# Optimization experiments

Hardware: AMD Instinct MI355X
Metric: run time of the kernel (lower is better)

The kernel has to match this reference:

```python
import jax, jax.numpy as jnp
import numpy as np

B, L, D = 8192, 2048, 256


def setup_inputs() -> dict:
    key = jax.random.key(0)
    kx, kl = jax.random.split(key)
    x = jax.random.normal(kx, (B, D), dtype=jnp.float32)
    landmarks = jax.random.normal(kl, (L, D), dtype=jnp.float32)
    return {"x": x, "landmarks": landmarks}


def reference(x, landmarks):
    # RBF layer: out[b, l] = exp(-gamma * sum_d (landmarks[l, d] - x[b, d])^2)
    # gamma='auto' -> 1 / n_features (landmarks.shape[1])
    gamma = jnp.float32(1.0 / landmarks.shape[1])
    # avoids materializing the [B, L, D] broadcast-diff intermediate)
    x2 = jnp.sum(x * x, axis=-1, keepdims=True)          # [B, 1]
    l2 = jnp.sum(landmarks * landmarks, axis=-1)         # [L]
    cross = jnp.einsum('bd,ld->bl', x, landmarks)        # [B, L]
    d2 = jnp.maximum(x2 + l2[None, :] - 2.0 * cross, 0.0)
    return jnp.exp(-gamma * d2)
```

## Files before the change

### kernel.cpp

```cpp
#include <hip/hip_runtime.h>


typedef __bf16 bf16x8 __attribute__((ext_vector_type(8)));
typedef float  f32x4  __attribute__((ext_vector_type(4)));

#define B_ROWS 8192
#define L_ROWS 2048
#define K_DIM  256

#define GLD_LDS(g, l) __builtin_amdgcn_global_load_lds(                      \
    (const __attribute__((address_space(1))) void*)(g),                      \
    (__attribute__((address_space(3))) void*)(l), 16, 0, 0)

__device__ __forceinline__ unsigned short f32_to_bf16_rne(float f) {
    union { float f; unsigned int u; } v; v.f = f;
    unsigned int u = v.u;
    unsigned int r = (u + 0x7fffu + ((u >> 16) & 1u)) >> 16;
    return (unsigned short)r;
}

__global__ __launch_bounds__(256) void cvt_rows_kernel(
    const float* __restrict__ x, const float* __restrict__ lm,
    unsigned short* __restrict__ xb, unsigned short* __restrict__ lb,
    float* __restrict__ x2, float* __restrict__ l2)
{
    const int lane = threadIdx.x & 63;
    const int gw   = blockIdx.x * 4 + (threadIdx.x >> 6);
    const float* in; unsigned short* outb; float* sq; int row;
    if (gw < B_ROWS) { in = x;  outb = xb; sq = x2; row = gw; }
    else             { in = lm; outb = lb; sq = l2; row = gw - B_ROWS; }
    const float4 v = ((const float4*)(in + (size_t)row * K_DIM))[lane];
    ushort4 o;
    o.x = f32_to_bf16_rne(v.x);
    o.y = f32_to_bf16_rne(v.y);
    o.z = f32_to_bf16_rne(v.z);
    o.w = f32_to_bf16_rne(v.w);
    ((ushort4*)(outb + (size_t)row * K_DIM))[lane] = o;
    float s = v.x*v.x + v.y*v.y + v.z*v.z + v.w*v.w;
    #pragma unroll
    for (int off = 32; off > 0; off >>= 1) s += __shfl_down(s, off, 64);
    if (lane == 0) sq[row] = s;
}

__global__ __launch_bounds__(512, 2) void rbf_gemm_kernel(
    const unsigned short* __restrict__ A,
    const unsigned short* __restrict__ Bm,
    const float* __restrict__ x2,
    const float* __restrict__ l2,
    float* __restrict__ out)
{
    __shared__ unsigned short As[2][256 * 64];
    __shared__ unsigned short Bs[2][256 * 64];

    const int tid  = threadIdx.x;
    const int wave = tid >> 6;
    const int lane = tid & 63;
    const int wm = wave >> 2;
    const int wn = wave & 3;

    const int bid = blockIdx.x;
    const int wg  = (bid & 7) * 32 + (bid >> 3);
    const int bm  = wg & 31;
    const int bn  = wg >> 5;

    f32x4 acc[8][4];
    #pragma unroll
    for (int i = 0; i < 8; ++i)
        #pragma unroll
        for (int j = 0; j < 4; ++j)
            acc[i][j] = (f32x4){0.f, 0.f, 0.f, 0.f};

    const int ldrow = lane >> 3;
    const int ldcol = (((lane & 7) ^ ldrow) * 8);

    const unsigned short* Ab = A  + (size_t)(bm * 256) * K_DIM;
    const unsigned short* Bb = Bm + (size_t)(bn * 256) * K_DIM;

#define STAGE(buf, k0)                                                       \
    _Pragma("unroll")                                                        \
    for (int it = 0; it < 4; ++it) {                                         \
        const int r = wave * 32 + it * 8;                                    \
        GLD_LDS(Ab + (r + ldrow) * K_DIM + (k0) + ldcol, &As[buf][r * 64]);  \
        GLD_LDS(Bb + (r + ldrow) * K_DIM + (k0) + ldcol, &Bs[buf][r * 64]);  \
    }

    STAGE(0, 0);

    const int xr = (lane & 7) << 4;

    #pragma unroll
    for (int t = 0; t < 4; ++t) {
        const int cur = t & 1;
        if (t < 3) { STAGE(cur ^ 1, (t + 1) * 64); }
        if (t < 3) asm volatile("s_waitcnt vmcnt(8)" ::: "memory");
        else       asm volatile("s_waitcnt vmcnt(0)" ::: "memory");
        asm volatile("s_barrier" ::: "memory");

        #pragma unroll
        for (int kk = 0; kk < 64; kk += 32) {
            const int osw = ((kk * 2 + (lane >> 4) * 16) ^ xr) >> 1;
            bf16x8 af[8], bfr[4];
            #pragma unroll
            for (int nt = 0; nt < 4; ++nt)
                bfr[nt] = *(const bf16x8*)&Bs[cur][(wn*64 + nt*16 + (lane & 15)) * 64 + osw];
            #pragma unroll
            for (int mt = 0; mt < 8; ++mt)
                af[mt]  = *(const bf16x8*)&As[cur][(wm*128 + mt*16 + (lane & 15)) * 64 + osw];
            #pragma unroll
            for (int mt = 0; mt < 8; ++mt)
                #pragma unroll
                for (int nt = 0; nt < 4; ++nt)
                    acc[mt][nt] = __builtin_amdgcn_mfma_f32_16x16x32_bf16(
                        bfr[nt], af[mt], acc[mt][nt], 0, 0, 0);
        }
        if (t < 3) asm volatile("s_barrier" ::: "memory");
    }
#undef STAGE

    const float gamma = 1.0f / 256.0f;
    const int row0 = bm * 256 + wm * 128 + (lane & 15);
    const int col0 = bn * 256 + wn * 64 + (lane >> 4) * 4;

    f32x4 lv[4];
    #pragma unroll
    for (int nt = 0; nt < 4; ++nt) lv[nt] = *(const f32x4*)&l2[col0 + nt * 16];

    #pragma unroll
    for (int mt = 0; mt < 8; ++mt) {
        const int row = row0 + mt * 16;
        const float xv = x2[row];
        const size_t rb = (size_t)row * L_ROWS;
        #pragma unroll
        for (int nt = 0; nt < 4; ++nt) {
            f32x4 v;
            #pragma unroll
            for (int r = 0; r < 4; ++r) {
                float d2 = fmaxf(xv + lv[nt][r] - 2.0f * acc[mt][nt][r], 0.0f);
                v[r] = __expf(-gamma * d2);
            }
            __builtin_nontemporal_store(v, (f32x4*)&out[rb + col0 + nt * 16]);
        }
    }
}

extern "C" void kernel_launch(void* const* d_in, const int* in_sizes, int n_in,
                              void* d_out, int out_size, void* d_ws, size_t ws_size,
                              hipStream_t stream) {
    const float* x  = (const float*)d_in[0];
    const float* lm = (const float*)d_in[1];
    float* out = (float*)d_out;

    char* ws = (char*)d_ws;
    unsigned short* xb = (unsigned short*)ws;
    unsigned short* lb = (unsigned short*)(ws + (size_t)B_ROWS*K_DIM*2);
    float* x2 = (float*)(ws + (size_t)B_ROWS*K_DIM*2 + (size_t)L_ROWS*K_DIM*2);
    float* l2 = x2 + B_ROWS;

    cvt_rows_kernel<<<(B_ROWS + L_ROWS)/4, 256, 0, stream>>>(x, lm, xb, lb, x2, l2);
    rbf_gemm_kernel<<<256, 512, 0, stream>>>(xb, lb, x2, l2, out);
}
```

Before: 98.31 us.

## Split GEMM main loop into four quadrant phases interleaving staging loads and MFMAs

The per-k-tile loop is restructured into four sub-phases. Each phase reads a quarter of the A/B fragments from LDS and issues a partial global-to-LDS stage of the next tile, then runs a block of MFMAs raised to higher priority with s_setprio. The intent is to spread memory traffic across the compute phases and shrink register footprint for fragments, hiding load latency behind matrix math. It adds many more barriers per tile and relies on hand-tuned vmcnt counts, which risks sync overhead or ordering mistakes.

```diff
diff --git a/kernel.cpp b/kernel.cpp
--- a/kernel.cpp
+++ b/kernel.cpp
@@ -76,46 +76,100 @@
     const unsigned short* Ab = A  + (size_t)(bm * 256) * K_DIM;
     const unsigned short* Bb = Bm + (size_t)(bn * 256) * K_DIM;
 
-#define STAGE(buf, k0)                                                       \
-    _Pragma("unroll")                                                        \
-    for (int it = 0; it < 4; ++it) {                                         \
-        const int r = wave * 32 + it * 8;                                    \
-        GLD_LDS(Ab + (r + ldrow) * K_DIM + (k0) + ldcol, &As[buf][r * 64]);  \
-        GLD_LDS(Bb + (r + ldrow) * K_DIM + (k0) + ldcol, &Bs[buf][r * 64]);  \
-    }
-
-    STAGE(0, 0);
+#define STAGE_A(buf, k0, h)                                                   \
+    _Pragma("unroll")                                                         \
+    for (int i = 0; i < 2; ++i) {                                             \
+        const int r = i * 128 + (h) * 64 + wave * 8;                          \
+        GLD_LDS(Ab + (r + ldrow) * K_DIM + (k0) + ldcol, &As[buf][r * 64]);   \
+    }
+#define STAGE_B(buf, k0, h)                                                   \
+    _Pragma("unroll")                                                         \
+    for (int i = 0; i < 2; ++i) {                                             \
+        const int r = i * 128 + (wave >> 2) * 64 + (h) * 32 + (wave & 3) * 8; \
+        GLD_LDS(Bb + (r + ldrow) * K_DIM + (k0) + ldcol, &Bs[buf][r * 64]);   \
+    }
+
+    STAGE_A(0, 0, 0);
+    STAGE_B(0, 0, 0);
+    STAGE_B(0, 0, 1);
+    STAGE_A(0, 0, 1);
+    asm volatile("s_waitcnt vmcnt(4)" ::: "memory");
+    asm volatile("s_barrier" ::: "memory");
 
     const int xr = (lane & 7) << 4;
+    const int osw0 = ((0  + (lane >> 4) * 16) ^ xr) >> 1;
+    const int osw1 = ((64 + (lane >> 4) * 16) ^ xr) >> 1;
+
+    bf16x8 af[4][2], bf0[2][2], bf1[2][2];
+
+#define RD_A(mh)                                                              \
+    _Pragma("unroll")                                                         \
+    for (int mt = 0; mt < 4; ++mt) {                                          \
+        const int rr = (wm * 128 + ((mh) * 4 + mt) * 16 + (lane & 15)) * 64;  \
+        af[mt][0] = *(const bf16x8*)&As[cur][rr + osw0];                      \
+        af[mt][1] = *(const bf16x8*)&As[cur][rr + osw1];                      \
+    }
+#define RD_B(dst, nh)                                                         \
+    _Pragma("unroll")                                                         \
+    for (int nt = 0; nt < 2; ++nt) {                                          \
+        const int rr = (wn * 64 + ((nh) * 2 + nt) * 16 + (lane & 15)) * 64;   \
+        dst[nt][0] = *(const bf16x8*)&Bs[cur][rr + osw0];                     \
+        dst[nt][1] = *(const bf16x8*)&Bs[cur][rr + osw1];                     \
+    }
+#define QUAD(mh, nh, bfx)                                                     \
+    __builtin_amdgcn_s_setprio(1);                                            \
+    _Pragma("unroll")                                                         \
+    for (int mt = 0; mt < 4; ++mt)                                            \
+        _Pragma("unroll")                                                     \
+        for (int nt = 0; nt < 2; ++nt)                                        \
+            _Pragma("unroll")                                                 \
+            for (int kk = 0; kk < 2; ++kk)                                    \
+                acc[(mh)*4+mt][(nh)*2+nt] =                                   \
+                    __builtin_amdgcn_mfma_f32_16x16x32_bf16(                  \
+                        bfx[nt][kk], af[mt][kk], acc[(mh)*4+mt][(nh)*2+nt],   \
+                        0, 0, 0);                                             \
+    __builtin_amdgcn_s_setprio(0);
+#define BAR asm volatile("s_barrier" ::: "memory")
 
     #pragma unroll
     for (int t = 0; t < 4; ++t) {
-        const int cur = t & 1;
-        if (t < 3) { STAGE(cur ^ 1, (t + 1) * 64); }
-        if (t < 3) asm volatile("s_waitcnt vmcnt(8)" ::: "memory");
-        else       asm volatile("s_waitcnt vmcnt(0)" ::: "memory");
-        asm volatile("s_barrier" ::: "memory");
-
-        #pragma unroll
-        for (int kk = 0; kk < 64; kk += 32) {
-            const int osw = ((kk * 2 + (lane >> 4) * 16) ^ xr) >> 1;
-            bf16x8 af[8], bfr[4];
-            #pragma unroll
-            for (int nt = 0; nt < 4; ++nt)
-                bfr[nt] = *(const bf16x8*)&Bs[cur][(wn*64 + nt*16 + (lane & 15)) * 64 + osw];
-            #pragma unroll
-            for (int mt = 0; mt < 8; ++mt)
-                af[mt]  = *(const bf16x8*)&As[cur][(wm*128 + mt*16 + (lane & 15)) * 64 + osw];
-            #pragma unroll
-            for (int mt = 0; mt < 8; ++mt)
-                #pragma unroll
-                for (int nt = 0; nt < 4; ++nt)
-                    acc[mt][nt] = __builtin_amdgcn_mfma_f32_16x16x32_bf16(
-                        bfr[nt], af[mt], acc[mt][nt], 0, 0, 0);
-        }
-        if (t < 3) asm volatile("s_barrier" ::: "memory");
-    }
-#undef STAGE
+        const int cur = t & 1, nxt = cur ^ 1;
+        const int k0n = (t + 1) * 64;
+
+        RD_A(0); RD_B(bf0, 0);
+        if (t < 3) { STAGE_A(nxt, k0n, 0);
+                     asm volatile("s_waitcnt vmcnt(4)" ::: "memory"); }
+        else       { asm volatile("s_waitcnt vmcnt(2)" ::: "memory"); }
+        BAR;
+        QUAD(0, 0, bf0);
+        BAR;
+
+        RD_B(bf1, 1);
+        if (t < 3) { STAGE_B(nxt, k0n, 0);
+                     asm volatile("s_waitcnt vmcnt(4)" ::: "memory"); }
+        else       { asm volatile("s_waitcnt vmcnt(0)" ::: "memory"); }
+        BAR;
+        QUAD(0, 1, bf1);
+        BAR;
+
+        RD_A(1);
+        if (t < 3) { STAGE_B(nxt, k0n, 1); }
+        BAR;
+        QUAD(1, 0, bf0);
+        BAR;
+
+        if (t < 3) { STAGE_A(nxt, k0n, 1);
+                     asm volatile("s_waitcnt vmcnt(4)" ::: "memory"); }
+        BAR;
+        QUAD(1, 1, bf1);
+        if (t < 3) BAR;
+    }
+#undef STAGE_A
+#undef STAGE_B
+#undef RD_A
+#undef RD_B
+#undef QUAD
+#undef BAR
 
     const float gamma = 1.0f / 256.0f;
     const int row0 = bm * 256 + wm * 128 + (lane & 15);
```

After: 100.3 us. +2.1%, slower.
